# Performance work log

Hardware: AMD Instinct MI355X
Metric: run time of the kernel (lower is better)

The kernel has to match this reference:

```python
import jax, jax.numpy as jnp
import numpy as np

BATCH, S, N_DIM, B_SIZE = 512, 66, 304, 128

def setup_inputs() -> dict:
    key = jax.random.key(0)
    kx, kw = jax.random.split(key)
    x = jax.random.normal(kx, (BATCH, S, N_DIM), dtype=jnp.float32)
    W = jax.random.normal(kw, (B_SIZE, N_DIM), dtype=jnp.float32) * (1.0 / np.sqrt(N_DIM))
    b = jnp.zeros((B_SIZE,), dtype=jnp.float32)
    return {"x": x, "W": W, "b": b}

def reference(x, W, b):
    # Linear projection into tree space: (batch, S, B_size)
    t = jnp.einsum('bsd,kd->bsk', x, W) + b
    # Pairwise squared distances over sentence positions, same math as
    # expand/transpose/subtract/pow(2)/sum in the torch module.
    diff = t[:, :, None, :] - t[:, None, :, :]        # (batch, S, S, B_size)
    return jnp.sum(diff * diff, axis=-1)               # (batch, S, S)
```

## Files before the change

### kernel.cpp

```cpp
#include <hip/hip_runtime.h>
#include <hip/hip_bf16.h>

#define NBATCH 512
#define NS 66
#define ND 304
#define NK 128

#define XROWS 80
#define XSTRIDE_B 640
#define XBYTES (XROWS * XSTRIDE_B)
#define TSTRIDE_B 256
#define TBYTES (XROWS * TSTRIDE_B)
#define NTHREADS 512

#define WCOLS 320
#define WBYTES (NK * WCOLS * 2)

typedef __attribute__((ext_vector_type(8))) short bf16x8;
typedef __attribute__((ext_vector_type(4))) short s16x4;
typedef __attribute__((ext_vector_type(4))) float f32x4;

__device__ __forceinline__ short f2bf(float x) {
    return __builtin_bit_cast(short, __float2bfloat16(x));
}

__device__ const int TI_LUT[15] = {0,1,2,3,4, 0,0,0,0,1,1,1,2,2,3};
__device__ const int TJ_LUT[15] = {0,1,2,3,4, 1,2,3,4,2,3,4,3,4,4};

__global__ __launch_bounds__(256) void wconvert(const float* __restrict__ W,
                                                short* __restrict__ Wb) {
    const int idx = blockIdx.x * 256 + threadIdx.x;
    if (idx >= NK * (WCOLS / 8)) return;
    const int r  = idx / (WCOLS / 8);
    const int c0 = (idx % (WCOLS / 8)) * 8;
    bf16x8 f = {0, 0, 0, 0, 0, 0, 0, 0};
    if (c0 < ND) {
        const float4 p0 = *reinterpret_cast<const float4*>(W + r * ND + c0);
        const float4 p1 = *reinterpret_cast<const float4*>(W + r * ND + c0 + 4);
        f[0] = f2bf(p0.x); f[1] = f2bf(p0.y); f[2] = f2bf(p0.z); f[3] = f2bf(p0.w);
        f[4] = f2bf(p1.x); f[5] = f2bf(p1.y); f[6] = f2bf(p1.z); f[7] = f2bf(p1.w);
    }
    *reinterpret_cast<bf16x8*>(Wb + r * WCOLS + c0) = f;
}

template <bool WPRE>
__global__ __launch_bounds__(NTHREADS, 4) void treeprobe_mfma(
    const float* __restrict__ x,
    const float* __restrict__ W,
    const short* __restrict__ Wb,
    float* __restrict__ out)
{
    __shared__ __align__(16) char lds[XBYTES + TBYTES + 80 * 4];
    char* const t_lds = lds + XBYTES;
    float* const norms = (float*)(lds + XBYTES + TBYTES);

    const int tid   = threadIdx.x;
    const int batch = blockIdx.x;
    const int lane  = tid & 63;
    const int wv    = tid >> 6;
    const int lr    = lane & 15;
    const int lg    = lane >> 4;

    const float* __restrict__ xb = x + (size_t)batch * NS * ND;

    float4 aA[6], aB[5];
#pragma unroll
    for (int i = 0; i < 6; ++i) {
        const int e = tid + i * NTHREADS;
        aA[i] = (e < 2640)
            ? *reinterpret_cast<const float4*>(xb + (e / 40) * ND + (e % 40) * 4)
            : make_float4(0.f, 0.f, 0.f, 0.f);
    }
#pragma unroll
    for (int i = 0; i < 5; ++i) {
        const int e = tid + i * NTHREADS;
        aB[i] = (e < 2376)
            ? *reinterpret_cast<const float4*>(xb + (e / 36) * ND + 160 + (e % 36) * 4)
            : make_float4(0.f, 0.f, 0.f, 0.f);
    }

    bf16x8 wfrag[10];
    const int wc = wv * 16 + lr;
    if constexpr (WPRE) {
#pragma unroll
        for (int kk = 0; kk < 10; ++kk)
            wfrag[kk] = *reinterpret_cast<const bf16x8*>(
                Wb + wc * WCOLS + kk * 32 + lg * 8);
    } else {
        const float* __restrict__ wr = W + wc * ND;
#pragma unroll
        for (int kk = 0; kk < 10; ++kk) {
            const int k0 = kk * 32 + lg * 8;
            bf16x8 f = {0, 0, 0, 0, 0, 0, 0, 0};
            if (k0 < ND) {
                const float4 p0 = *reinterpret_cast<const float4*>(wr + k0);
                const float4 p1 = *reinterpret_cast<const float4*>(wr + k0 + 4);
                f[0] = f2bf(p0.x); f[1] = f2bf(p0.y);
                f[2] = f2bf(p0.z); f[3] = f2bf(p0.w);
                f[4] = f2bf(p1.x); f[5] = f2bf(p1.y);
                f[6] = f2bf(p1.z); f[7] = f2bf(p1.w);
            }
            wfrag[kk] = f;
        }
    }

    for (int i = tid; i < 560; i += NTHREADS) {
        const int row = 66 + i / 40;
        *reinterpret_cast<f32x4*>(lds + row * XSTRIDE_B + (i % 40) * 16) =
            (f32x4){0.f, 0.f, 0.f, 0.f};
    }
    for (int i = tid; i < 132; i += NTHREADS) {
        const int row = i >> 1;
        const int byte = (row * XSTRIDE_B + 608 + (i & 1) * 16) ^ ((row & 7) << 4);
        *reinterpret_cast<f32x4*>(lds + byte) = (f32x4){0.f, 0.f, 0.f, 0.f};
    }

#pragma unroll
    for (int i = 0; i < 6; ++i) {
        const int e = tid + i * NTHREADS;
        if (e < 2640) {
            const int s = e / 40;
            const int f = (e % 40) * 4;
            const int byte = (s * XSTRIDE_B + f * 2) ^ ((s & 7) << 4);
            s16x4 sv;
            sv[0] = f2bf(aA[i].x); sv[1] = f2bf(aA[i].y);
            sv[2] = f2bf(aA[i].z); sv[3] = f2bf(aA[i].w);
            *reinterpret_cast<s16x4*>(lds + byte) = sv;
        }
    }
#pragma unroll
    for (int i = 0; i < 5; ++i) {
        const int e = tid + i * NTHREADS;
        if (e < 2376) {
            const int s = e / 36;
            const int f = 160 + (e % 36) * 4;
            const int byte = (s * XSTRIDE_B + f * 2) ^ ((s & 7) << 4);
            s16x4 sv;
            sv[0] = f2bf(aB[i].x); sv[1] = f2bf(aB[i].y);
            sv[2] = f2bf(aB[i].z); sv[3] = f2bf(aB[i].w);
            *reinterpret_cast<s16x4*>(lds + byte) = sv;
        }
    }
    __syncthreads();

    f32x4 acc[5];
#pragma unroll
    for (int st = 0; st < 5; ++st) acc[st] = (f32x4){0.f, 0.f, 0.f, 0.f};

#pragma unroll
    for (int kk = 0; kk < 10; ++kk) {
        bf16x8 a[5];
#pragma unroll
        for (int st = 0; st < 5; ++st) {
            const int row = st * 16 + lr;
            const int byte = (row * XSTRIDE_B + kk * 64 + lg * 16) ^ ((row & 7) << 4);
            a[st] = *reinterpret_cast<const bf16x8*>(lds + byte);
        }
#pragma unroll
        for (int st = 0; st < 5; ++st)
            acc[st] = __builtin_amdgcn_mfma_f32_16x16x32_bf16(
                wfrag[kk], a[st], acc[st], 0, 0, 0);
    }

#pragma unroll
    for (int st = 0; st < 5; ++st) {
        const int s = st * 16 + lr;
        const int c0 = wv * 16 + lg * 4;
        const int byte = (s * TSTRIDE_B + c0 * 2) ^ ((s & 7) << 4);
        s16x4 sv;
        sv[0] = f2bf(acc[st][0]); sv[1] = f2bf(acc[st][1]);
        sv[2] = f2bf(acc[st][2]); sv[3] = f2bf(acc[st][3]);
        *reinterpret_cast<s16x4*>(t_lds + byte) = sv;
    }
    __syncthreads();

    const int idx0 = wv;
    const int idx1 = wv + 8;
    const int ti0 = TI_LUT[idx0], tj0 = TJ_LUT[idx0];

    f32x4 g0 = (f32x4){0.f, 0.f, 0.f, 0.f};
#pragma unroll
    for (int kk = 0; kk < 4; ++kk) {
        const int ra = ti0 * 16 + lr;
        const int ba = (ra * TSTRIDE_B + kk * 64 + lg * 16) ^ ((ra & 7) << 4);
        const int rb = tj0 * 16 + lr;
        const int bb = (rb * TSTRIDE_B + kk * 64 + lg * 16) ^ ((rb & 7) << 4);
        g0 = __builtin_amdgcn_mfma_f32_16x16x32_bf16(
            *reinterpret_cast<const bf16x8*>(t_lds + ba),
            *reinterpret_cast<const bf16x8*>(t_lds + bb), g0, 0, 0, 0);
    }
    if (wv < 5) {
#pragma unroll
        for (int r = 0; r < 4; ++r)
            if (lr == lg * 4 + r) norms[wv * 16 + lr] = g0[r];
    }

    f32x4 g1 = (f32x4){0.f, 0.f, 0.f, 0.f};
    int ti1 = 0, tj1 = 0;
    if (idx1 < 15) {
        ti1 = TI_LUT[idx1]; tj1 = TJ_LUT[idx1];
#pragma unroll
        for (int kk = 0; kk < 4; ++kk) {
            const int ra = ti1 * 16 + lr;
            const int ba = (ra * TSTRIDE_B + kk * 64 + lg * 16) ^ ((ra & 7) << 4);
            const int rb = tj1 * 16 + lr;
            const int bb = (rb * TSTRIDE_B + kk * 64 + lg * 16) ^ ((rb & 7) << 4);
            g1 = __builtin_amdgcn_mfma_f32_16x16x32_bf16(
                *reinterpret_cast<const bf16x8*>(t_lds + ba),
                *reinterpret_cast<const bf16x8*>(t_lds + bb), g1, 0, 0, 0);
        }
    }
    __syncthreads();

    float* __restrict__ ob = out + (size_t)batch * NS * NS;

    {
        const int j = tj0 * 16 + lr;
        const float nj = norms[j];
        float v[4];
#pragma unroll
        for (int r = 0; r < 4; ++r) {
            const int i = ti0 * 16 + lg * 4 + r;
            v[r] = norms[i] + nj - 2.f * g0[r];
            if (i < NS && j < NS) ob[i * NS + j] = v[r];
        }
        if (ti0 != tj0 && j < NS) {
            const int i0 = ti0 * 16 + lg * 4;
            *reinterpret_cast<float2*>(ob + j * NS + i0)     = make_float2(v[0], v[1]);
            *reinterpret_cast<float2*>(ob + j * NS + i0 + 2) = make_float2(v[2], v[3]);
        }
    }
    if (idx1 < 15) {
        const int j = tj1 * 16 + lr;
        const float nj = norms[j];
        float v[4];
#pragma unroll
        for (int r = 0; r < 4; ++r) {
            const int i = ti1 * 16 + lg * 4 + r;
            v[r] = norms[i] + nj - 2.f * g1[r];
            if (i < NS && j < NS) ob[i * NS + j] = v[r];
        }
        if (j < NS) {
            const int i0 = ti1 * 16 + lg * 4;
            *reinterpret_cast<float2*>(ob + j * NS + i0)     = make_float2(v[0], v[1]);
            *reinterpret_cast<float2*>(ob + j * NS + i0 + 2) = make_float2(v[2], v[3]);
        }
    }
}

extern "C" void kernel_launch(void* const* d_in, const int* in_sizes, int n_in,
                              void* d_out, int out_size, void* d_ws, size_t ws_size,
                              hipStream_t stream) {
    const float* x = (const float*)d_in[0];
    const float* W = (const float*)d_in[1];
    float* out = (float*)d_out;

    if (ws_size >= (size_t)WBYTES) {
        short* Wb = (short*)d_ws;
        wconvert<<<(NK * (WCOLS / 8) + 255) / 256, 256, 0, stream>>>(W, Wb);
        treeprobe_mfma<true><<<NBATCH, NTHREADS, 0, stream>>>(x, W, Wb, out);
    } else {
        treeprobe_mfma<false><<<NBATCH, NTHREADS, 0, stream>>>(x, W, nullptr, out);
    }
}
```

Measured before the change: 24.12 us.

## Drop W pre-convert kernel and pipeline x staging with per-row-tile MFMA

Removes the separate W-to-bf16 conversion kernel and converts W fragments inline from fp32 loads, saving one launch. The x tile is now loaded as contiguous 76-float4 rows in one pass, and the bf16 conversion and LDS writes are split into five groups, each followed by a barrier and that row-tile's MFMA chain, so compute on early rows overlaps the later conversions. __syncthreads is replaced by a raw lgkmcnt wait plus s_barrier. In exchange there are more barriers, higher register pressure from holding 20 fp32 W vectors and 10 x vectors, and the hand-written barrier depends on correct waitcnt semantics.

After: 25.63 us. 1.06x slower.

```diff
diff --git a/kernel.cpp b/kernel.cpp
--- a/kernel.cpp
+++ b/kernel.cpp
@@ -5,16 +5,12 @@
 #define NS 66
 #define ND 304
 #define NK 128
-
-#define XROWS 80
+#define NTHREADS 512
+
 #define XSTRIDE_B 640
-#define XBYTES (XROWS * XSTRIDE_B)
+#define XBYTES (80 * XSTRIDE_B)
 #define TSTRIDE_B 256
-#define TBYTES (XROWS * TSTRIDE_B)
-#define NTHREADS 512
-
-#define WCOLS 320
-#define WBYTES (NK * WCOLS * 2)
+#define TBYTES (80 * TSTRIDE_B)
 
 typedef __attribute__((ext_vector_type(8))) short bf16x8;
 typedef __attribute__((ext_vector_type(4))) short s16x4;
@@ -27,27 +23,11 @@
 __device__ const int TI_LUT[15] = {0,1,2,3,4, 0,0,0,0,1,1,1,2,2,3};
 __device__ const int TJ_LUT[15] = {0,1,2,3,4, 1,2,3,4,2,3,4,3,4,4};
 
-__global__ __launch_bounds__(256) void wconvert(const float* __restrict__ W,
-                                                short* __restrict__ Wb) {
-    const int idx = blockIdx.x * 256 + threadIdx.x;
-    if (idx >= NK * (WCOLS / 8)) return;
-    const int r  = idx / (WCOLS / 8);
-    const int c0 = (idx % (WCOLS / 8)) * 8;
-    bf16x8 f = {0, 0, 0, 0, 0, 0, 0, 0};
-    if (c0 < ND) {
-        const float4 p0 = *reinterpret_cast<const float4*>(W + r * ND + c0);
-        const float4 p1 = *reinterpret_cast<const float4*>(W + r * ND + c0 + 4);
-        f[0] = f2bf(p0.x); f[1] = f2bf(p0.y); f[2] = f2bf(p0.z); f[3] = f2bf(p0.w);
-        f[4] = f2bf(p1.x); f[5] = f2bf(p1.y); f[6] = f2bf(p1.z); f[7] = f2bf(p1.w);
-    }
-    *reinterpret_cast<bf16x8*>(Wb + r * WCOLS + c0) = f;
-}
-
-template <bool WPRE>
+#define LDS_BARRIER() asm volatile("s_waitcnt lgkmcnt(0)\n\ts_barrier" ::: "memory")
+
 __global__ __launch_bounds__(NTHREADS, 4) void treeprobe_mfma(
     const float* __restrict__ x,
     const float* __restrict__ W,
-    const short* __restrict__ Wb,
     float* __restrict__ out)
 {
     __shared__ __align__(16) char lds[XBYTES + TBYTES + 80 * 4];
@@ -63,45 +43,34 @@
 
     const float* __restrict__ xb = x + (size_t)batch * NS * ND;
 
-    float4 aA[6], aB[5];
-#pragma unroll
-    for (int i = 0; i < 6; ++i) {
-        const int e = tid + i * NTHREADS;
-        aA[i] = (e < 2640)
-            ? *reinterpret_cast<const float4*>(xb + (e / 40) * ND + (e % 40) * 4)
+    float4 ax[10];
+
+#pragma unroll
+    for (int g = 0; g < 3; ++g) {
+        const int e = g * NTHREADS + tid;
+        ax[g] = *reinterpret_cast<const float4*>(xb + (e / 76) * ND + (e % 76) * 4);
+    }
+
+    const int wc = wv * 16 + lr;
+    const float* __restrict__ wr = W + wc * ND;
+    float4 wp[20];
+#pragma unroll
+    for (int kk = 0; kk < 10; ++kk) {
+        const int k0 = kk * 32 + lg * 8;
+        if (k0 < ND) {
+            wp[kk * 2]     = *reinterpret_cast<const float4*>(wr + k0);
+            wp[kk * 2 + 1] = *reinterpret_cast<const float4*>(wr + k0 + 4);
+        } else {
+            wp[kk * 2] = wp[kk * 2 + 1] = make_float4(0.f, 0.f, 0.f, 0.f);
+        }
+    }
+
+#pragma unroll
+    for (int g = 3; g < 10; ++g) {
+        const int e = g * NTHREADS + tid;
+        ax[g] = (e < 5016)
+            ? *reinterpret_cast<const float4*>(xb + (e / 76) * ND + (e % 76) * 4)
             : make_float4(0.f, 0.f, 0.f, 0.f);
-    }
-#pragma unroll
-    for (int i = 0; i < 5; ++i) {
-        const int e = tid + i * NTHREADS;
-        aB[i] = (e < 2376)
-            ? *reinterpret_cast<const float4*>(xb + (e / 36) * ND + 160 + (e % 36) * 4)
-            : make_float4(0.f, 0.f, 0.f, 0.f);
-    }
-
-    bf16x8 wfrag[10];
-    const int wc = wv * 16 + lr;
-    if constexpr (WPRE) {
-#pragma unroll
-        for (int kk = 0; kk < 10; ++kk)
-            wfrag[kk] = *reinterpret_cast<const bf16x8*>(
-                Wb + wc * WCOLS + kk * 32 + lg * 8);
-    } else {
-        const float* __restrict__ wr = W + wc * ND;
-#pragma unroll
-        for (int kk = 0; kk < 10; ++kk) {
-            const int k0 = kk * 32 + lg * 8;
-            bf16x8 f = {0, 0, 0, 0, 0, 0, 0, 0};
-            if (k0 < ND) {
-                const float4 p0 = *reinterpret_cast<const float4*>(wr + k0);
-                const float4 p1 = *reinterpret_cast<const float4*>(wr + k0 + 4);
-                f[0] = f2bf(p0.x); f[1] = f2bf(p0.y);
-                f[2] = f2bf(p0.z); f[3] = f2bf(p0.w);
-                f[4] = f2bf(p1.x); f[5] = f2bf(p1.y);
-                f[6] = f2bf(p1.z); f[7] = f2bf(p1.w);
-            }
-            wfrag[kk] = f;
-        }
     }
 
     for (int i = tid; i < 560; i += NTHREADS) {
@@ -115,51 +84,50 @@
         *reinterpret_cast<f32x4*>(lds + byte) = (f32x4){0.f, 0.f, 0.f, 0.f};
     }
 
-#pragma unroll
-    for (int i = 0; i < 6; ++i) {
-        const int e = tid + i * NTHREADS;
-        if (e < 2640) {
-            const int s = e / 40;
-            const int f = (e % 40) * 4;
-            const int byte = (s * XSTRIDE_B + f * 2) ^ ((s & 7) << 4);
-            s16x4 sv;
-            sv[0] = f2bf(aA[i].x); sv[1] = f2bf(aA[i].y);
-            sv[2] = f2bf(aA[i].z); sv[3] = f2bf(aA[i].w);
-            *reinterpret_cast<s16x4*>(lds + byte) = sv;
-        }
-    }
-#pragma unroll
-    for (int i = 0; i < 5; ++i) {
-        const int e = tid + i * NTHREADS;
-        if (e < 2376) {
-            const int s = e / 36;
-            const int f = 160 + (e % 36) * 4;
-            const int byte = (s * XSTRIDE_B + f * 2) ^ ((s & 7) << 4);
-            s16x4 sv;
-            sv[0] = f2bf(aB[i].x); sv[1] = f2bf(aB[i].y);
-            sv[2] = f2bf(aB[i].z); sv[3] = f2bf(aB[i].w);
-            *reinterpret_cast<s16x4*>(lds + byte) = sv;
-        }
-    }
-    __syncthreads();
+    bf16x8 wfrag[10];
+#pragma unroll
+    for (int kk = 0; kk < 10; ++kk) {
+        bf16x8 f;
+        f[0] = f2bf(wp[kk * 2].x);     f[1] = f2bf(wp[kk * 2].y);
+        f[2] = f2bf(wp[kk * 2].z);     f[3] = f2bf(wp[kk * 2].w);
+        f[4] = f2bf(wp[kk * 2 + 1].x); f[5] = f2bf(wp[kk * 2 + 1].y);
+        f[6] = f2bf(wp[kk * 2 + 1].z); f[7] = f2bf(wp[kk * 2 + 1].w);
+        wfrag[kk] = f;
+    }
 
     f32x4 acc[5];
 #pragma unroll
     for (int st = 0; st < 5; ++st) acc[st] = (f32x4){0.f, 0.f, 0.f, 0.f};
 
 #pragma unroll
-    for (int kk = 0; kk < 10; ++kk) {
-        bf16x8 a[5];
-#pragma unroll
-        for (int st = 0; st < 5; ++st) {
-            const int row = st * 16 + lr;
+    for (int m = 0; m < 5; ++m) {
+        const int GS[5] = {0, 3, 5, 8, 10};
+        const int GE[5] = {3, 5, 8, 10, 10};
+#pragma unroll
+        for (int g = 0; g < 10; ++g) {
+            if (g >= GS[m] && g < GE[m]) {
+                const int e = g * NTHREADS + tid;
+                if (e < 5016) {
+                    const int s = e / 76;
+                    const int c = (e % 76) * 4;
+                    const int byte = (s * XSTRIDE_B + c * 2) ^ ((s & 7) << 4);
+                    s16x4 sv;
+                    sv[0] = f2bf(ax[g].x); sv[1] = f2bf(ax[g].y);
+                    sv[2] = f2bf(ax[g].z); sv[3] = f2bf(ax[g].w);
+                    *reinterpret_cast<s16x4*>(lds + byte) = sv;
+                }
+            }
+        }
+        LDS_BARRIER();
+
+#pragma unroll
+        for (int kk = 0; kk < 10; ++kk) {
+            const int row = m * 16 + lr;
             const int byte = (row * XSTRIDE_B + kk * 64 + lg * 16) ^ ((row & 7) << 4);
-            a[st] = *reinterpret_cast<const bf16x8*>(lds + byte);
-        }
-#pragma unroll
-        for (int st = 0; st < 5; ++st)
-            acc[st] = __builtin_amdgcn_mfma_f32_16x16x32_bf16(
-                wfrag[kk], a[st], acc[st], 0, 0, 0);
+            const bf16x8 a = *reinterpret_cast<const bf16x8*>(lds + byte);
+            acc[m] = __builtin_amdgcn_mfma_f32_16x16x32_bf16(
+                wfrag[kk], a, acc[m], 0, 0, 0);
+        }
     }
 
 #pragma unroll
@@ -172,7 +140,7 @@
         sv[2] = f2bf(acc[st][2]); sv[3] = f2bf(acc[st][3]);
         *reinterpret_cast<s16x4*>(t_lds + byte) = sv;
     }
-    __syncthreads();
+    LDS_BARRIER();
 
     const int idx0 = wv;
     const int idx1 = wv + 8;
@@ -210,7 +178,7 @@
                 *reinterpret_cast<const bf16x8*>(t_lds + bb), g1, 0, 0, 0);
         }
     }
-    __syncthreads();
+    LDS_BARRIER();
 
     float* __restrict__ ob = out + (size_t)batch * NS * NS;
 
@@ -255,11 +223,5 @@
     const float* W = (const float*)d_in[1];
     float* out = (float*)d_out;
 
-    if (ws_size >= (size_t)WBYTES) {
-        short* Wb = (short*)d_ws;
-        wconvert<<<(NK * (WCOLS / 8) + 255) / 256, 256, 0, stream>>>(W, Wb);
-        treeprobe_mfma<true><<<NBATCH, NTHREADS, 0, stream>>>(x, W, Wb, out);
-    } else {
-        treeprobe_mfma<false><<<NBATCH, NTHREADS, 0, stream>>>(x, W, nullptr, out);
-    }
+    treeprobe_mfma<<<NBATCH, NTHREADS, 0, stream>>>(x, W, out);
 }
```
